# Performance work log

Measured on AMD Instinct MI355X. Metric: run time of the kernel, lower is better.

Reference implementation:

```python
import jax, jax.numpy as jnp
import numpy as np

# YOLOLayer config (matches init_kwargs)
ANCHORS = [(0.1, 0.13), (0.3, 0.35), (0.6, 0.55)]  # (w, h) as fraction of image
NUM_CLASSES = 80
STRIDE = 8
NA = len(ANCHORS)


def setup_inputs() -> dict:
    key = jax.random.key(0)
    B, C, G = 16, NA * (NUM_CLASSES + 5), 64
    x = jax.random.normal(key, (B, C, G, G), dtype=jnp.float32)
    return {"x": x}


def reference(x):
    B = x.shape[0]
    g0, g1 = x.shape[2], x.shape[3]
    nC = NUM_CLASSES
    # [B, nA, g0, g1, 5+nC]
    pred = x.reshape(B, NA, nC + 5, g0, g1).transpose(0, 1, 3, 4, 2)
    sx = jax.nn.sigmoid(pred[..., 0])
    sy = jax.nn.sigmoid(pred[..., 1])
    w = pred[..., 2]
    h = pred[..., 3]
    pred_conf = jax.nn.sigmoid(pred[..., 4])
    pred_cls = jax.nn.sigmoid(pred[..., 5:])

    # grid offsets: grid_x varies along last dim, grid_y along dim -2 (torch semantics)
    grid_x = jnp.arange(g1, dtype=x.dtype)[None, None, None, :]
    grid_y = jnp.arange(g0, dtype=x.dtype)[None, None, :, None]
    scaled = jnp.asarray([(aw * g0, ah * g1) for aw, ah in ANCHORS], dtype=x.dtype)
    anchor_w = scaled[:, 0].reshape(1, NA, 1, 1)
    anchor_h = scaled[:, 1].reshape(1, NA, 1, 1)

    # torch uses .data (detached) for pred_boxes -> stop_gradient for faithfulness
    pred_boxes = jnp.stack(
        [sx + grid_x, sy + grid_y, jnp.exp(w) * anchor_w, jnp.exp(h) * anchor_h],
        axis=-1,
    )
    pred_boxes = jax.lax.stop_gradient(pred_boxes)

    boxes = pred_boxes.reshape(B, -1, 4) * STRIDE
    conf = pred_conf.reshape(B, -1, 1)
    cls = pred_cls.reshape(B, -1, nC)
    return boxes, conf, cls
```

## Files before the change

### kernel.cpp

```cpp
#include <hip/hip_runtime.h>


#define NB 16
#define NA 3
#define NC 80
#define GG 4096
#define CH 85

__device__ __forceinline__ float sigmoidf(float v) {
    return 1.0f / (1.0f + __expf(-v));
}

__global__ __launch_bounds__(256) void yolo_kernel(const float* __restrict__ x,
                                                   float* __restrict__ out) {
    constexpr int S = 64;
    __shared__ float lds[CH][S + 1];

    const int tilesPer = GG / S;
    int blk  = blockIdx.x;
    int tile = blk % tilesPer;
    int ba   = blk / tilesPer;
    int a    = ba % NA;
    int s0   = tile * S;

    const float* __restrict__ xin = x + (size_t)ba * CH * GG + s0;
    for (int i = threadIdx.x; i < CH * S; i += 256) {
        int ch = i >> 6;
        int p  = i & 63;
        lds[ch][p] = xin[(size_t)ch * GG + p];
    }
    __syncthreads();

    const float anchor_w[NA] = {0.1f * 64 * 8, 0.3f * 64 * 8, 0.6f * 64 * 8};
    const float anchor_h[NA] = {0.13f * 64 * 8, 0.35f * 64 * 8, 0.55f * 64 * 8};

    const int loc = ba * GG + s0;
    float* __restrict__ boxes = out;
    float* __restrict__ conf  = out + (size_t)NB * NA * GG * 4;
    float* __restrict__ cls   = out + (size_t)NB * NA * GG * 5;

    if (threadIdx.x < S) {
        int p  = threadIdx.x;
        int sp = s0 + p;
        float gx = (float)(sp & 63);
        float gy = (float)(sp >> 6);
        float4 bx;
        bx.x = (sigmoidf(lds[0][p]) + gx) * 8.0f;
        bx.y = (sigmoidf(lds[1][p]) + gy) * 8.0f;
        bx.z = __expf(lds[2][p]) * anchor_w[a];
        bx.w = __expf(lds[3][p]) * anchor_h[a];
        reinterpret_cast<float4*>(boxes)[loc + p] = bx;
        conf[loc + p] = sigmoidf(lds[4][p]);
    }

    float* __restrict__ clsBase = cls + (size_t)loc * NC;
    for (int i = threadIdx.x; i < NC * S; i += 256) {
        int p = i / NC;
        int c = i - p * NC;
        clsBase[i] = sigmoidf(lds[5 + c][p]);
    }
}

extern "C" void kernel_launch(void* const* d_in, const int* in_sizes, int n_in,
                              void* d_out, int out_size, void* d_ws, size_t ws_size,
                              hipStream_t stream) {
    const float* x = (const float*)d_in[0];
    float* out = (float*)d_out;
    dim3 grid(NB * NA * (GG / 64));
    yolo_kernel<<<grid, 256, 0, stream>>>(x, out);
}
```

Baseline: 28.95 us.

## Vectorize loads/stores with float4 and swizzled LDS, enlarge tile to 128

Result: faster. 27.44 us (-5.2%).

```diff
diff --git a/kernel.cpp b/kernel.cpp
--- a/kernel.cpp
+++ b/kernel.cpp
@@ -6,28 +6,36 @@
 #define NC 80
 #define GG 4096
 #define CH 85
+#define S  128
 
 __device__ __forceinline__ float sigmoidf(float v) {
     return 1.0f / (1.0f + __expf(-v));
 }
 
-__global__ __launch_bounds__(256) void yolo_kernel(const float* __restrict__ x,
+__device__ __forceinline__ int lidx(int ch, int p) {
+    int g = (p >> 2) ^ ((ch >> 2) & 7);
+    return ch * S + (g << 2) + (p & 3);
+}
+
+__global__ __launch_bounds__(512) void yolo_kernel(const float* __restrict__ x,
                                                    float* __restrict__ out) {
-    constexpr int S = 64;
-    __shared__ float lds[CH][S + 1];
+    __shared__ float lds[CH * S];
 
     const int tilesPer = GG / S;
     int blk  = blockIdx.x;
-    int tile = blk % tilesPer;
+    int tile = blk & (tilesPer - 1);
     int ba   = blk / tilesPer;
     int a    = ba % NA;
     int s0   = tile * S;
 
-    const float* __restrict__ xin = x + (size_t)ba * CH * GG + s0;
-    for (int i = threadIdx.x; i < CH * S; i += 256) {
-        int ch = i >> 6;
-        int p  = i & 63;
-        lds[ch][p] = xin[(size_t)ch * GG + p];
+    const float4* __restrict__ xin4 =
+        reinterpret_cast<const float4*>(x + (size_t)ba * CH * GG + s0);
+    for (int i = threadIdx.x; i < CH * (S / 4); i += 512) {
+        int ch = i >> 5;
+        int p4 = i & 31;
+        int g  = p4 ^ ((ch >> 2) & 7);
+        float4 v = xin4[ch * (GG / 4) + p4];
+        *reinterpret_cast<float4*>(&lds[ch * S + (g << 2)]) = v;
     }
     __syncthreads();
 
@@ -45,19 +53,26 @@
         float gx = (float)(sp & 63);
         float gy = (float)(sp >> 6);
         float4 bx;
-        bx.x = (sigmoidf(lds[0][p]) + gx) * 8.0f;
-        bx.y = (sigmoidf(lds[1][p]) + gy) * 8.0f;
-        bx.z = __expf(lds[2][p]) * anchor_w[a];
-        bx.w = __expf(lds[3][p]) * anchor_h[a];
+        bx.x = (sigmoidf(lds[lidx(0, p)]) + gx) * 8.0f;
+        bx.y = (sigmoidf(lds[lidx(1, p)]) + gy) * 8.0f;
+        bx.z = __expf(lds[lidx(2, p)]) * anchor_w[a];
+        bx.w = __expf(lds[lidx(3, p)]) * anchor_h[a];
         reinterpret_cast<float4*>(boxes)[loc + p] = bx;
-        conf[loc + p] = sigmoidf(lds[4][p]);
+        conf[loc + p] = sigmoidf(lds[lidx(4, p)]);
     }
 
-    float* __restrict__ clsBase = cls + (size_t)loc * NC;
-    for (int i = threadIdx.x; i < NC * S; i += 256) {
-        int p = i / NC;
-        int c = i - p * NC;
-        clsBase[i] = sigmoidf(lds[5 + c][p]);
+    float4* __restrict__ cls4 =
+        reinterpret_cast<float4*>(cls + (size_t)loc * NC);
+    for (int i = threadIdx.x; i < NC * (S / 4); i += 512) {
+        int p  = i / 20;
+        int c4 = i % 20;
+        int r  = 5 + (c4 << 2);
+        float4 v;
+        v.x = sigmoidf(lds[lidx(r + 0, p)]);
+        v.y = sigmoidf(lds[lidx(r + 1, p)]);
+        v.z = sigmoidf(lds[lidx(r + 2, p)]);
+        v.w = sigmoidf(lds[lidx(r + 3, p)]);
+        cls4[i] = v;
     }
 }
 
@@ -66,6 +81,6 @@
                               hipStream_t stream) {
     const float* x = (const float*)d_in[0];
     float* out = (float*)d_out;
-    dim3 grid(NB * NA * (GG / 64));
-    yolo_kernel<<<grid, 256, 0, stream>>>(x, out);
+    dim3 grid(NB * NA * (GG / S));
+    yolo_kernel<<<grid, 512, 0, stream>>>(x, out);
 }
```

## Replace LDS transpose with register-level 4x4 transposes and float4 I/O

Applied to the files above, without the earlier changes.

Measured after the change: 53.43 us. +84.6%, slower.

```diff
diff --git a/kernel.cpp b/kernel.cpp
--- a/kernel.cpp
+++ b/kernel.cpp
@@ -11,53 +11,71 @@
     return 1.0f / (1.0f + __expf(-v));
 }
 
-__global__ __launch_bounds__(256) void yolo_kernel(const float* __restrict__ x,
+__global__ __launch_bounds__(128) void yolo_kernel(const float* __restrict__ x,
                                                    float* __restrict__ out) {
-    constexpr int S = 64;
-    __shared__ float lds[CH][S + 1];
+    const int blk  = blockIdx.x;
+    const int tile = blk & 15;
+    const int ba   = blk >> 4;
+    const int a    = ba % NA;
+    const int lane = threadIdx.x & 63;
+    const int wv   = threadIdx.x >> 6;
+    const int p0   = tile * 256 + lane * 4;
 
-    const int tilesPer = GG / S;
-    int blk  = blockIdx.x;
-    int tile = blk % tilesPer;
-    int ba   = blk / tilesPer;
-    int a    = ba % NA;
-    int s0   = tile * S;
+    const float* __restrict__ xin = x + (size_t)ba * CH * GG + p0;
+    const int loc0 = ba * GG + p0;
 
-    const float* __restrict__ xin = x + (size_t)ba * CH * GG + s0;
-    for (int i = threadIdx.x; i < CH * S; i += 256) {
-        int ch = i >> 6;
-        int p  = i & 63;
-        lds[ch][p] = xin[(size_t)ch * GG + p];
-    }
-    __syncthreads();
+    float4* __restrict__ boxes4 = reinterpret_cast<float4*>(out);
+    float*  __restrict__ conf   = out + (size_t)NB * NA * GG * 4;
+    float4* __restrict__ cls4   =
+        reinterpret_cast<float4*>(out + (size_t)NB * NA * GG * 5);
 
-    const float anchor_w[NA] = {0.1f * 64 * 8, 0.3f * 64 * 8, 0.6f * 64 * 8};
-    const float anchor_h[NA] = {0.13f * 64 * 8, 0.35f * 64 * 8, 0.55f * 64 * 8};
-
-    const int loc = ba * GG + s0;
-    float* __restrict__ boxes = out;
-    float* __restrict__ conf  = out + (size_t)NB * NA * GG * 4;
-    float* __restrict__ cls   = out + (size_t)NB * NA * GG * 5;
-
-    if (threadIdx.x < S) {
-        int p  = threadIdx.x;
-        int sp = s0 + p;
-        float gx = (float)(sp & 63);
-        float gy = (float)(sp >> 6);
-        float4 bx;
-        bx.x = (sigmoidf(lds[0][p]) + gx) * 8.0f;
-        bx.y = (sigmoidf(lds[1][p]) + gy) * 8.0f;
-        bx.z = __expf(lds[2][p]) * anchor_w[a];
-        bx.w = __expf(lds[3][p]) * anchor_h[a];
-        reinterpret_cast<float4*>(boxes)[loc + p] = bx;
-        conf[loc + p] = sigmoidf(lds[4][p]);
+    int k0, k1;
+    if (wv == 0) {
+        const float anchor_w[NA] = {0.1f * 64 * 8, 0.3f * 64 * 8, 0.6f * 64 * 8};
+        const float anchor_h[NA] = {0.13f * 64 * 8, 0.35f * 64 * 8, 0.55f * 64 * 8};
+        float4 c0 = *reinterpret_cast<const float4*>(xin + 0 * GG);
+        float4 c1 = *reinterpret_cast<const float4*>(xin + 1 * GG);
+        float4 c2 = *reinterpret_cast<const float4*>(xin + 2 * GG);
+        float4 c3 = *reinterpret_cast<const float4*>(xin + 3 * GG);
+        float4 c4 = *reinterpret_cast<const float4*>(xin + 4 * GG);
+        const float aw = anchor_w[a], ah = anchor_h[a];
+        #pragma unroll
+        for (int q = 0; q < 4; ++q) {
+            int p = p0 + q;
+            float gx = (float)(p & 63);
+            float gy = (float)(p >> 6);
+            float4 bx;
+            bx.x = (sigmoidf(reinterpret_cast<float*>(&c0)[q]) + gx) * 8.0f;
+            bx.y = (sigmoidf(reinterpret_cast<float*>(&c1)[q]) + gy) * 8.0f;
+            bx.z = __expf(reinterpret_cast<float*>(&c2)[q]) * aw;
+            bx.w = __expf(reinterpret_cast<float*>(&c3)[q]) * ah;
+            boxes4[loc0 + q] = bx;
+        }
+        float4 cf;
+        cf.x = sigmoidf(c4.x); cf.y = sigmoidf(c4.y);
+        cf.z = sigmoidf(c4.z); cf.w = sigmoidf(c4.w);
+        *reinterpret_cast<float4*>(conf + loc0) = cf;
+        k0 = 0;  k1 = 10;
+    } else {
+        k0 = 10; k1 = 20;
     }
 
-    float* __restrict__ clsBase = cls + (size_t)loc * NC;
-    for (int i = threadIdx.x; i < NC * S; i += 256) {
-        int p = i / NC;
-        int c = i - p * NC;
-        clsBase[i] = sigmoidf(lds[5 + c][p]);
+    #pragma unroll 2
+    for (int k = k0; k < k1; ++k) {
+        const float* chp = xin + (size_t)(5 + 4 * k) * GG;
+        float4 d0 = *reinterpret_cast<const float4*>(chp + 0 * GG);
+        float4 d1 = *reinterpret_cast<const float4*>(chp + 1 * GG);
+        float4 d2 = *reinterpret_cast<const float4*>(chp + 2 * GG);
+        float4 d3 = *reinterpret_cast<const float4*>(chp + 3 * GG);
+        #pragma unroll
+        for (int q = 0; q < 4; ++q) {
+            float4 v;
+            v.x = sigmoidf(reinterpret_cast<float*>(&d0)[q]);
+            v.y = sigmoidf(reinterpret_cast<float*>(&d1)[q]);
+            v.z = sigmoidf(reinterpret_cast<float*>(&d2)[q]);
+            v.w = sigmoidf(reinterpret_cast<float*>(&d3)[q]);
+            cls4[(size_t)(loc0 + q) * 20 + k] = v;
+        }
     }
 }
 
@@ -66,6 +84,6 @@
                               hipStream_t stream) {
     const float* x = (const float*)d_in[0];
     float* out = (float*)d_out;
-    dim3 grid(NB * NA * (GG / 64));
-    yolo_kernel<<<grid, 256, 0, stream>>>(x, out);
+    dim3 grid(NB * NA * (GG / 256));
+    yolo_kernel<<<grid, 128, 0, stream>>>(x, out);
 }
```
